# Optimization experiments

Measured on AMD Instinct MI355X. Metric: run time of the kernel, lower is better.

The kernel has to match this reference:

```python
import jax, jax.numpy as jnp
import numpy as np

BETA = 0.25


def setup_inputs() -> dict:
    key = jax.random.key(0)
    k1, k2 = jax.random.split(key)
    z_e = jax.random.normal(k1, (16, 64, 64, 64), dtype=jnp.float32)  # (B, D, H, W)
    embedding = jax.random.normal(k2, (1024, 64), dtype=jnp.float32)  # (K, D)
    return {"z_e": z_e, "embedding": embedding}


def reference(z_e, embedding):
    B, D, H, W = z_e.shape
    # (B, D, H, W) -> (B, H, W, D) -> (N, D)
    flat = jnp.transpose(z_e, (0, 2, 3, 1)).reshape(-1, D)
    # squared L2 distances to codebook: (N, K)
    dist = (jnp.sum(flat * flat, axis=1, keepdims=True)
            + jnp.sum(embedding * embedding, axis=1)
            - 2.0 * flat @ embedding.T)
    indices = jnp.argmin(dist, axis=1)  # (N,)
    z_q_flat = embedding[indices]  # (N, D) gather
    z_q = jnp.transpose(z_q_flat.reshape(B, H, W, D), (0, 3, 1, 2))  # (B, D, H, W)
    codebook_loss = jnp.mean((jax.lax.stop_gradient(z_q) - z_e) ** 2)
    commit_loss = jnp.mean((z_q - jax.lax.stop_gradient(z_e)) ** 2)
    vq_loss = codebook_loss + BETA * commit_loss
    # straight-through estimator
    z_q_st = z_e + jax.lax.stop_gradient(z_q - z_e)
    return (z_q_st, vq_loss, indices.reshape(B, H, W))
```

## Files before the change

kernel.cpp:

```cpp
#include <hip/hip_runtime.h>
#include <math.h>

typedef short  short8 __attribute__((ext_vector_type(8)));
typedef float  f32x4  __attribute__((ext_vector_type(4)));

#define ZQ_ELEMS 4194304
#define KC       1024
#define EPS_HALF 0.005f
#define PXB      128


__device__ inline unsigned short bf16_rne(float f) {
    union { float fv; unsigned u; } a; a.fv = f;
    unsigned r = a.u + 0x7FFFu + ((a.u >> 16) & 1u);
    return (unsigned short)(r >> 16);
}
__device__ inline float bf16_to_f(unsigned short h) {
    union { unsigned u; float fv; } a; a.u = ((unsigned)h) << 16;
    return a.fv;
}
__device__ inline double dpack(float hi, unsigned lo) {
    return __hiloint2double(__float_as_int(hi), (int)lo);
}
__device__ inline float dhi(double d) { return __int_as_float(__double2hiint(d)); }
__device__ inline unsigned dlo(double d) { return (unsigned)__double2loint(d); }

__global__ __launch_bounds__(256) void vq_prep(const float* __restrict__ emb,
        unsigned short* __restrict__ epack, float* __restrict__ enorm,
        int* __restrict__ risky_cnt, float* __restrict__ out) {
    const int k = blockIdx.x * 256 + threadIdx.x;
    if (k == 0) { *risky_cnt = 0; out[ZQ_ELEMS] = 0.f; }
    const float4* e4 = (const float4*)(emb + k * 64);
    float s = 0.f;
#pragma unroll
    for (int j = 0; j < 16; ++j) {
        float4 v = e4[j];
        float vv[4] = {v.x, v.y, v.z, v.w};
        ushort4 hv, lv;
        unsigned short h[4], l[4];
#pragma unroll
        for (int t = 0; t < 4; ++t) {
            s = fmaf(vv[t], vv[t], s);
            h[t] = bf16_rne(vv[t]);
            l[t] = bf16_rne(vv[t] - bf16_to_f(h[t]));
        }
        hv.x = h[0]; hv.y = h[1]; hv.z = h[2]; hv.w = h[3];
        lv.x = l[0]; lv.y = l[1]; lv.z = l[2]; lv.w = l[3];
        *(ushort4*)(epack + k * 128 + j * 4)      = hv;
        *(ushort4*)(epack + k * 128 + 64 + j * 4) = lv;
    }
    enorm[k] = s;
}

__global__ __launch_bounds__(256) void vq_scan(const float* __restrict__ z_e,
        const unsigned short* __restrict__ epack, const float* __restrict__ enorm,
        double* __restrict__ pbest, float* __restrict__ pb2) {
    const int tid  = threadIdx.x;
    const int lane = tid & 63;
    const int col  = lane & 15;
    const int g    = lane >> 4;
    const int wv   = __builtin_amdgcn_readfirstlane(tid >> 6);
    const int pxblock = blockIdx.x >> 2;
    const int grp     = blockIdx.x & 3;
    const int cbase   = grp * 256 + wv * 64;
    const int pblk    = pxblock * PXB;

    __shared__ __align__(16) char smem[32768];
    unsigned short* afrag = (unsigned short*)smem;
    double* mrgB = (double*)smem;
    float*  mrgS = (float*)(smem + 4096);

    {
        const int lp   = tid & 127;
        const int half = tid >> 7;
        const int pg   = pblk + lp;
        const float* zb = z_e + (pg >> 12) * 262144 + (pg & 4095);
        const int sx = (lp & 7) << 3;
#pragma unroll
        for (int s8 = 0; s8 < 4; ++s8) {
            const int d0 = half * 32 + s8 * 8;
            short8 H, L;
#pragma unroll
            for (int j = 0; j < 8; ++j) {
                float v = zb[(d0 + j) * 4096];
                unsigned short h = bf16_rne(v);
                H[j] = (short)h;
                L[j] = (short)bf16_rne(v - bf16_to_f(h));
            }
            const int sw = d0 ^ sx;
            *(short8*)&afrag[lp * 128 + sw]      = H;
            *(short8*)&afrag[lp * 128 + 64 + sw] = L;
        }
    }

    short8 ah[4][2], al[4][2];
    f32x4 enf[4];
    int clo[4][4];
    const int K1 = 1023 - cbase - g * 4;
#pragma unroll
    for (int t = 0; t < 4; ++t) {
        const int code = cbase + t * 16 + col;
        const short8* ph = (const short8*)(epack + code * 128) + g;
        ah[t][0] = ph[0]; ah[t][1] = ph[4];
        al[t][0] = ph[8]; al[t][1] = ph[12];
        const float4 e4 = *(const float4*)(enorm + cbase + t * 16 + g * 4);
        enf[t][0] = -0.5f * e4.x; enf[t][1] = -0.5f * e4.y;
        enf[t][2] = -0.5f * e4.z; enf[t][3] = -0.5f * e4.w;
#pragma unroll
        for (int r = 0; r < 4; ++r) clo[t][r] = K1 - t * 16 - r;
    }
    __syncthreads();

    const f32x4 zero4 = {0.f, 0.f, 0.f, 0.f};
    const int g8 = g * 8;

    double Brun[8];
    float  Srun[8];
#pragma unroll
    for (int it = 0; it < 8; ++it) { Brun[it] = dpack(-INFINITY, 0u); Srun[it] = -INFINITY; }

#pragma unroll
    for (int it = 0; it < 8; ++it) {
        const int lpx = it * 16 + col;
        const int sxp = (lpx & 7) << 3;
        const unsigned short* ap = &afrag[lpx * 128];
        const short8 bh0 = *(const short8*)&ap[(g8        ) ^ sxp];
        const short8 bh1 = *(const short8*)&ap[(32 + g8   ) ^ sxp];
        const short8 bl0 = *(const short8*)&ap[64 + ((g8     ) ^ sxp)];
        const short8 bl1 = *(const short8*)&ap[64 + ((32 + g8) ^ sxp)];

        double B = Brun[it];
        float  S = Srun[it];
#pragma unroll
        for (int t = 0; t < 4; ++t) {
            f32x4 aA, aB;
            aA = __builtin_amdgcn_mfma_f32_16x16x32_bf16(ah[t][0], bh0, enf[t], 0, 0, 0);
            aB = __builtin_amdgcn_mfma_f32_16x16x32_bf16(ah[t][1], bh1, zero4, 0, 0, 0);
            aA = __builtin_amdgcn_mfma_f32_16x16x32_bf16(al[t][0], bh0, aA, 0, 0, 0);
            aB = __builtin_amdgcn_mfma_f32_16x16x32_bf16(al[t][1], bh1, aB, 0, 0, 0);
            aA = __builtin_amdgcn_mfma_f32_16x16x32_bf16(ah[t][0], bl0, aA, 0, 0, 0);
            aB = __builtin_amdgcn_mfma_f32_16x16x32_bf16(ah[t][1], bl1, aB, 0, 0, 0);
#pragma unroll
            for (int r = 0; r < 4; ++r) {
                const float v = aA[r] + aB[r];
                S = __builtin_amdgcn_fmed3f(dhi(B), S, v);
                B = fmax(B, dpack(v, (unsigned)clo[t][r]));
            }
        }
        Brun[it] = B;
        Srun[it] = S;
    }

#pragma unroll
    for (int it = 0; it < 8; ++it) {
        double B = Brun[it];
        float  S = Srun[it];
#pragma unroll
        for (int s = 16; s < 64; s <<= 1) {
            const double ob = __shfl_xor(B, s, 64);
            const float  o2 = __shfl_xor(S, s, 64);
            S = __builtin_amdgcn_fmed3f(dhi(B), dhi(ob), fmaxf(S, o2));
            B = fmax(B, ob);
        }
        Brun[it] = B;
        Srun[it] = S;
    }

    __syncthreads();
    if (g == 0) {
#pragma unroll
        for (int it = 0; it < 8; ++it) {
            mrgB[wv * PXB + it * 16 + col] = Brun[it];
            mrgS[wv * PXB + it * 16 + col] = Srun[it];
        }
    }
    __syncthreads();

    if (tid < PXB) {
        double B = mrgB[tid];
        float  S = mrgS[tid];
#pragma unroll
        for (int w = 1; w < 4; ++w) {
            const double ob = mrgB[w * PXB + tid];
            const float  o2 = mrgS[w * PXB + tid];
            S = __builtin_amdgcn_fmed3f(dhi(B), dhi(ob), fmaxf(S, o2));
            B = fmax(B, ob);
        }
        const int pxg = pblk + tid;
        pbest[grp * 65536 + pxg] = B;
        pb2[grp * 65536 + pxg]   = S;
    }
}

__global__ __launch_bounds__(256) void vq_final(const float* __restrict__ z_e,
        const float* __restrict__ emb, const double* __restrict__ pbest,
        const float* __restrict__ pb2, float* __restrict__ out,
        int* __restrict__ risky_cnt, int* __restrict__ risky) {
    __shared__ float zq[64][65];
    __shared__ int   sidx[64];
    __shared__ float sred[4];
    const int tid  = threadIdx.x;
    const int lane = tid & 63;
    const int w    = __builtin_amdgcn_readfirstlane(tid >> 6);
    const int pblk = blockIdx.x * 64;
    const int batch = pblk >> 12;
    const int hw0   = pblk & 4095;

    if (w == 0) {
        const int px = pblk + lane;
        double B = pbest[px];
        float  S = pb2[px];
#pragma unroll
        for (int gq = 1; gq < 4; ++gq) {
            const double ob = pbest[gq * 65536 + px];
            const float  o2 = pb2[gq * 65536 + px];
            S = __builtin_amdgcn_fmed3f(dhi(B), dhi(ob), fmaxf(S, o2));
            B = fmax(B, ob);
        }
        const int idx = 1023 - (int)dlo(B);
        sidx[lane] = idx;
        out[ZQ_ELEMS + 1 + px] = (float)idx;
        const bool risk = (dhi(B) - S < EPS_HALF);
        const unsigned long long m = __ballot(risk);
        int base = 0;
        if (lane == 0 && m) base = atomicAdd(risky_cnt, __popcll(m));
        base = __shfl(base, 0, 64);
        if (risk) risky[base + __popcll(m & ((1ull << lane) - 1ull))] = px;
    }
    __syncthreads();

#pragma unroll
    for (int i = 0; i < 16; ++i) {
        const int p = w * 16 + i;
        const int k = sidx[p];
        zq[p][lane] = emb[k * 64 + lane];
    }
    __syncthreads();

    const int p4 = (tid & 15) * 4;
    const float* zeb = z_e + batch * 262144 + hw0;
    float* ob = out + batch * 262144 + hw0;
    float ss = 0.f;
#pragma unroll
    for (int it = 0; it < 4; ++it) {
        const int d = (tid >> 4) + it * 16;
        float4 q;
        q.x = zq[p4 + 0][d]; q.y = zq[p4 + 1][d];
        q.z = zq[p4 + 2][d]; q.w = zq[p4 + 3][d];
        const float4 z = *(const float4*)(zeb + d * 4096 + p4);
        *(float4*)(ob + d * 4096 + p4) = q;
        const float e0 = q.x - z.x, e1 = q.y - z.y, e2 = q.z - z.z, e3 = q.w - z.w;
        ss += e0 * e0 + e1 * e1 + e2 * e2 + e3 * e3;
    }
    for (int off = 32; off; off >>= 1) ss += __shfl_down(ss, off, 64);
    if (lane == 0) sred[w] = ss;
    __syncthreads();
    if (tid == 0)
        atomicAdd(out + ZQ_ELEMS,
                  ((sred[0] + sred[1]) + (sred[2] + sred[3])) * (1.25f / (float)ZQ_ELEMS));
}

__global__ __launch_bounds__(256) void vq_fix(const float* __restrict__ z_e,
        const float* __restrict__ emb, float* __restrict__ out,
        const int* __restrict__ cnt, const int* __restrict__ list) {
    const int n = *cnt;
    if ((int)blockIdx.x * 4 >= n) return;
    __shared__ float etile[64][65];
    const int tid  = threadIdx.x;
    const int lane = tid & 63;
    const int wv   = __builtin_amdgcn_readfirstlane(tid >> 6);

    for (int base = blockIdx.x * 4; base < n; base += gridDim.x * 4) {
        const int item = base + wv;
        const bool active = item < n;
        int pix = 0, oldk = 0;
        float f[64];
        if (active) {
            pix = list[item];
            const float* zb = z_e + (pix >> 12) * 262144 + (pix & 4095);
#pragma unroll
            for (int d = 0; d < 64; ++d) f[d] = zb[d * 4096];
            oldk = (int)out[ZQ_ELEMS + 1 + pix];
        }
        double best = INFINITY; int bk = KC;
        double dold = 0.0;
        for (int j = 0; j < 16; ++j) {
            __syncthreads();
#pragma unroll
            for (int i = 0; i < 16; ++i) {
                const int idx = i * 256 + tid;
                etile[idx >> 6][idx & 63] = emb[j * 4096 + idx];
            }
            __syncthreads();
            if (active) {
                const int k = j * 64 + lane;
                double a0 = 0.0, a1 = 0.0;
#pragma unroll
                for (int d = 0; d < 64; d += 2) {
                    const double d0 = (double)f[d]     - (double)etile[lane][d];
                    const double d1 = (double)f[d + 1] - (double)etile[lane][d + 1];
                    a0 = fma(d0, d0, a0);
                    a1 = fma(d1, d1, a1);
                }
                const double acc = a0 + a1;
                if (acc < best || (acc == best && k < bk)) { best = acc; bk = k; }
                if (k == oldk) dold = acc;
            }
        }
        if (active) {
            for (int off = 32; off; off >>= 1) {
                const double ov = __shfl_down(best, off, 64);
                const int    oi = __shfl_down(bk, off, 64);
                if (ov < best || (ov == best && oi < bk)) { best = ov; bk = oi; }
            }
            for (int off = 32; off; off >>= 1) dold += __shfl_down(dold, off, 64);
            bk   = __shfl(bk, 0, 64);
            best = __shfl(best, 0, 64);
            dold = __shfl(dold, 0, 64);
            if (bk != oldk) {
                if (lane == 0) out[ZQ_ELEMS + 1 + pix] = (float)bk;
                out[(pix >> 12) * 262144 + (pix & 4095) + lane * 4096] = emb[bk * 64 + lane];
                if (lane == 0)
                    atomicAdd(out + ZQ_ELEMS,
                              (float)((best - dold) * (1.25 / (double)ZQ_ELEMS)));
            }
        }
    }
}

extern "C" void kernel_launch(void* const* d_in, const int* in_sizes, int n_in,
                              void* d_out, int out_size, void* d_ws, size_t ws_size,
                              hipStream_t stream) {
    const float* z_e = (const float*)d_in[0];
    const float* emb = (const float*)d_in[1];
    float* out = (float*)d_out;
    char* ws = (char*)d_ws;
    unsigned short* epack = (unsigned short*)ws;
    float*  enorm     = (float*)(ws + 262144);
    int*    risky_cnt = (int*)(ws + 266240);
    int*    risky     = (int*)(ws + 270336);
    double* pbest     = (double*)(ws + 524288);
    float*  pb2       = (float*)(ws + 2621440);

    vq_prep<<<4, 256, 0, stream>>>(emb, epack, enorm, risky_cnt, out);
    vq_scan<<<2048, 256, 0, stream>>>(z_e, epack, enorm, pbest, pb2);
    vq_final<<<1024, 256, 0, stream>>>(z_e, emb, pbest, pb2, out, risky_cnt, risky);
    vq_fix<<<512, 256, 0, stream>>>(z_e, emb, out, risky_cnt, risky);
}
```

Before: 90.03 us.

## Fuse scan and finalize kernels, looping over all codebook groups per block

Each block now handles 64 pixels against the full 1024-entry codebook in four sequential passes instead of splitting the codebook across four blocks. This lets the argmin merge, index write, risky-pixel listing, z_q gather, output write and loss reduction run in the same kernel, removing the pbest/pb2 global round trip and one kernel launch. In exchange, each pass reloads codebook fragments into registers, the grid halves to 1024 blocks, and per-block work becomes longer and more serialized.

```diff
diff --git a/kernel.cpp b/kernel.cpp
--- a/kernel.cpp
+++ b/kernel.cpp
@@ -7,7 +7,6 @@
 #define ZQ_ELEMS 4194304
 #define KC       1024
 #define EPS_HALF 0.005f
-#define PXB      128
 
 
 __device__ inline unsigned short bf16_rne(float f) {
@@ -54,31 +53,31 @@
 
 __global__ __launch_bounds__(256) void vq_scan(const float* __restrict__ z_e,
         const unsigned short* __restrict__ epack, const float* __restrict__ enorm,
-        double* __restrict__ pbest, float* __restrict__ pb2) {
+        const float* __restrict__ emb, float* __restrict__ out,
+        int* __restrict__ risky_cnt, int* __restrict__ risky) {
     const int tid  = threadIdx.x;
     const int lane = tid & 63;
     const int col  = lane & 15;
     const int g    = lane >> 4;
     const int wv   = __builtin_amdgcn_readfirstlane(tid >> 6);
-    const int pxblock = blockIdx.x >> 2;
-    const int grp     = blockIdx.x & 3;
-    const int cbase   = grp * 256 + wv * 64;
-    const int pblk    = pxblock * PXB;
-
-    __shared__ __align__(16) char smem[32768];
+    const int pblk = blockIdx.x * 64;
+
+    __shared__ __align__(16) char smem[19456];
     unsigned short* afrag = (unsigned short*)smem;
-    double* mrgB = (double*)smem;
-    float*  mrgS = (float*)(smem + 4096);
+    double* mrgB = (double*)(smem + 16384);
+    float*  mrgS = (float*)(smem + 18432);
+    float (*zq)[65] = (float (*)[65])smem;
+    __shared__ int   sidx[64];
+    __shared__ float sred[4];
 
     {
-        const int lp   = tid & 127;
-        const int half = tid >> 7;
-        const int pg   = pblk + lp;
+        const int lp = tid & 63;
+        const int pg = pblk + lp;
         const float* zb = z_e + (pg >> 12) * 262144 + (pg & 4095);
         const int sx = (lp & 7) << 3;
 #pragma unroll
-        for (int s8 = 0; s8 < 4; ++s8) {
-            const int d0 = half * 32 + s8 * 8;
+        for (int s8 = 0; s8 < 2; ++s8) {
+            const int d0 = wv * 16 + s8 * 8;
             short8 H, L;
 #pragma unroll
             for (int j = 0; j < 8; ++j) {
@@ -92,67 +91,68 @@
             *(short8*)&afrag[lp * 128 + 64 + sw] = L;
         }
     }
-
-    short8 ah[4][2], al[4][2];
-    f32x4 enf[4];
-    int clo[4][4];
-    const int K1 = 1023 - cbase - g * 4;
-#pragma unroll
-    for (int t = 0; t < 4; ++t) {
-        const int code = cbase + t * 16 + col;
-        const short8* ph = (const short8*)(epack + code * 128) + g;
-        ah[t][0] = ph[0]; ah[t][1] = ph[4];
-        al[t][0] = ph[8]; al[t][1] = ph[12];
-        const float4 e4 = *(const float4*)(enorm + cbase + t * 16 + g * 4);
-        enf[t][0] = -0.5f * e4.x; enf[t][1] = -0.5f * e4.y;
-        enf[t][2] = -0.5f * e4.z; enf[t][3] = -0.5f * e4.w;
-#pragma unroll
-        for (int r = 0; r < 4; ++r) clo[t][r] = K1 - t * 16 - r;
-    }
     __syncthreads();
 
     const f32x4 zero4 = {0.f, 0.f, 0.f, 0.f};
     const int g8 = g * 8;
 
-    double Brun[8];
-    float  Srun[8];
-#pragma unroll
-    for (int it = 0; it < 8; ++it) { Brun[it] = dpack(-INFINITY, 0u); Srun[it] = -INFINITY; }
-
-#pragma unroll
-    for (int it = 0; it < 8; ++it) {
-        const int lpx = it * 16 + col;
-        const int sxp = (lpx & 7) << 3;
-        const unsigned short* ap = &afrag[lpx * 128];
-        const short8 bh0 = *(const short8*)&ap[(g8        ) ^ sxp];
-        const short8 bh1 = *(const short8*)&ap[(32 + g8   ) ^ sxp];
-        const short8 bl0 = *(const short8*)&ap[64 + ((g8     ) ^ sxp)];
-        const short8 bl1 = *(const short8*)&ap[64 + ((32 + g8) ^ sxp)];
-
-        double B = Brun[it];
-        float  S = Srun[it];
+    double Brun[4];
+    float  Srun[4];
+#pragma unroll
+    for (int it = 0; it < 4; ++it) { Brun[it] = dpack(-INFINITY, 0u); Srun[it] = -INFINITY; }
+
+#pragma unroll 1
+    for (int pass = 0; pass < 4; ++pass) {
+        const int cbase = pass * 256 + wv * 64;
+        short8 ah[4][2], al[4][2];
+        f32x4 enf[4];
 #pragma unroll
         for (int t = 0; t < 4; ++t) {
-            f32x4 aA, aB;
-            aA = __builtin_amdgcn_mfma_f32_16x16x32_bf16(ah[t][0], bh0, enf[t], 0, 0, 0);
-            aB = __builtin_amdgcn_mfma_f32_16x16x32_bf16(ah[t][1], bh1, zero4, 0, 0, 0);
-            aA = __builtin_amdgcn_mfma_f32_16x16x32_bf16(al[t][0], bh0, aA, 0, 0, 0);
-            aB = __builtin_amdgcn_mfma_f32_16x16x32_bf16(al[t][1], bh1, aB, 0, 0, 0);
-            aA = __builtin_amdgcn_mfma_f32_16x16x32_bf16(ah[t][0], bl0, aA, 0, 0, 0);
-            aB = __builtin_amdgcn_mfma_f32_16x16x32_bf16(ah[t][1], bl1, aB, 0, 0, 0);
-#pragma unroll
-            for (int r = 0; r < 4; ++r) {
-                const float v = aA[r] + aB[r];
-                S = __builtin_amdgcn_fmed3f(dhi(B), S, v);
-                B = fmax(B, dpack(v, (unsigned)clo[t][r]));
-            }
-        }
-        Brun[it] = B;
-        Srun[it] = S;
-    }
-
-#pragma unroll
-    for (int it = 0; it < 8; ++it) {
+            const int code = cbase + t * 16 + col;
+            const short8* ph = (const short8*)(epack + code * 128) + g;
+            ah[t][0] = ph[0]; ah[t][1] = ph[4];
+            al[t][0] = ph[8]; al[t][1] = ph[12];
+            const float4 e4 = *(const float4*)(enorm + cbase + t * 16 + g * 4);
+            enf[t][0] = -0.5f * e4.x; enf[t][1] = -0.5f * e4.y;
+            enf[t][2] = -0.5f * e4.z; enf[t][3] = -0.5f * e4.w;
+        }
+        const int K1 = 1023 - cbase - g * 4;
+
+#pragma unroll
+        for (int it = 0; it < 4; ++it) {
+            const int lpx = it * 16 + col;
+            const int sxp = (lpx & 7) << 3;
+            const unsigned short* ap = &afrag[lpx * 128];
+            const short8 bh0 = *(const short8*)&ap[(g8     ) ^ sxp];
+            const short8 bh1 = *(const short8*)&ap[(32 + g8) ^ sxp];
+            const short8 bl0 = *(const short8*)&ap[64 + ((g8     ) ^ sxp)];
+            const short8 bl1 = *(const short8*)&ap[64 + ((32 + g8) ^ sxp)];
+
+            double B = Brun[it];
+            float  S = Srun[it];
+#pragma unroll
+            for (int t = 0; t < 4; ++t) {
+                f32x4 aA, aB;
+                aA = __builtin_amdgcn_mfma_f32_16x16x32_bf16(ah[t][0], bh0, enf[t], 0, 0, 0);
+                aB = __builtin_amdgcn_mfma_f32_16x16x32_bf16(ah[t][1], bh1, zero4, 0, 0, 0);
+                aA = __builtin_amdgcn_mfma_f32_16x16x32_bf16(al[t][0], bh0, aA, 0, 0, 0);
+                aB = __builtin_amdgcn_mfma_f32_16x16x32_bf16(al[t][1], bh1, aB, 0, 0, 0);
+                aA = __builtin_amdgcn_mfma_f32_16x16x32_bf16(ah[t][0], bl0, aA, 0, 0, 0);
+                aB = __builtin_amdgcn_mfma_f32_16x16x32_bf16(ah[t][1], bl1, aB, 0, 0, 0);
+#pragma unroll
+                for (int r = 0; r < 4; ++r) {
+                    const float v = aA[r] + aB[r];
+                    S = __builtin_amdgcn_fmed3f(dhi(B), S, v);
+                    B = fmax(B, dpack(v, (unsigned)(K1 - t * 16 - r)));
+                }
+            }
+            Brun[it] = B;
+            Srun[it] = S;
+        }
+    }
+
+#pragma unroll
+    for (int it = 0; it < 4; ++it) {
         double B = Brun[it];
         float  S = Srun[it];
 #pragma unroll
@@ -165,78 +165,48 @@
         Brun[it] = B;
         Srun[it] = S;
     }
-
     __syncthreads();
     if (g == 0) {
 #pragma unroll
-        for (int it = 0; it < 8; ++it) {
-            mrgB[wv * PXB + it * 16 + col] = Brun[it];
-            mrgS[wv * PXB + it * 16 + col] = Srun[it];
-        }
-    }
-    __syncthreads();
-
-    if (tid < PXB) {
+        for (int it = 0; it < 4; ++it) {
+            mrgB[wv * 64 + it * 16 + col] = Brun[it];
+            mrgS[wv * 64 + it * 16 + col] = Srun[it];
+        }
+    }
+    __syncthreads();
+
+    if (tid < 64) {
         double B = mrgB[tid];
         float  S = mrgS[tid];
 #pragma unroll
         for (int w = 1; w < 4; ++w) {
-            const double ob = mrgB[w * PXB + tid];
-            const float  o2 = mrgS[w * PXB + tid];
+            const double ob = mrgB[w * 64 + tid];
+            const float  o2 = mrgS[w * 64 + tid];
             S = __builtin_amdgcn_fmed3f(dhi(B), dhi(ob), fmaxf(S, o2));
             B = fmax(B, ob);
         }
-        const int pxg = pblk + tid;
-        pbest[grp * 65536 + pxg] = B;
-        pb2[grp * 65536 + pxg]   = S;
-    }
-}
-
-__global__ __launch_bounds__(256) void vq_final(const float* __restrict__ z_e,
-        const float* __restrict__ emb, const double* __restrict__ pbest,
-        const float* __restrict__ pb2, float* __restrict__ out,
-        int* __restrict__ risky_cnt, int* __restrict__ risky) {
-    __shared__ float zq[64][65];
-    __shared__ int   sidx[64];
-    __shared__ float sred[4];
-    const int tid  = threadIdx.x;
-    const int lane = tid & 63;
-    const int w    = __builtin_amdgcn_readfirstlane(tid >> 6);
-    const int pblk = blockIdx.x * 64;
-    const int batch = pblk >> 12;
-    const int hw0   = pblk & 4095;
-
-    if (w == 0) {
-        const int px = pblk + lane;
-        double B = pbest[px];
-        float  S = pb2[px];
-#pragma unroll
-        for (int gq = 1; gq < 4; ++gq) {
-            const double ob = pbest[gq * 65536 + px];
-            const float  o2 = pb2[gq * 65536 + px];
-            S = __builtin_amdgcn_fmed3f(dhi(B), dhi(ob), fmaxf(S, o2));
-            B = fmax(B, ob);
-        }
         const int idx = 1023 - (int)dlo(B);
-        sidx[lane] = idx;
-        out[ZQ_ELEMS + 1 + px] = (float)idx;
+        sidx[tid] = idx;
+        out[ZQ_ELEMS + 1 + pblk + tid] = (float)idx;
         const bool risk = (dhi(B) - S < EPS_HALF);
         const unsigned long long m = __ballot(risk);
         int base = 0;
         if (lane == 0 && m) base = atomicAdd(risky_cnt, __popcll(m));
         base = __shfl(base, 0, 64);
-        if (risk) risky[base + __popcll(m & ((1ull << lane) - 1ull))] = px;
+        if (risk) risky[base + __popcll(m & ((1ull << lane) - 1ull))] = pblk + tid;
     }
     __syncthreads();
 
 #pragma unroll
     for (int i = 0; i < 16; ++i) {
-        const int p = w * 16 + i;
+        const int p = wv * 16 + i;
         const int k = sidx[p];
         zq[p][lane] = emb[k * 64 + lane];
     }
     __syncthreads();
 
+    const int batch = pblk >> 12;
+    const int hw0   = pblk & 4095;
     const int p4 = (tid & 15) * 4;
     const float* zeb = z_e + batch * 262144 + hw0;
     float* ob = out + batch * 262144 + hw0;
@@ -253,7 +223,7 @@
         ss += e0 * e0 + e1 * e1 + e2 * e2 + e3 * e3;
     }
     for (int off = 32; off; off >>= 1) ss += __shfl_down(ss, off, 64);
-    if (lane == 0) sred[w] = ss;
+    if (lane == 0) sred[wv] = ss;
     __syncthreads();
     if (tid == 0)
         atomicAdd(out + ZQ_ELEMS,
@@ -339,11 +309,8 @@
     float*  enorm     = (float*)(ws + 262144);
     int*    risky_cnt = (int*)(ws + 266240);
     int*    risky     = (int*)(ws + 270336);
-    double* pbest     = (double*)(ws + 524288);
-    float*  pb2       = (float*)(ws + 2621440);
 
     vq_prep<<<4, 256, 0, stream>>>(emb, epack, enorm, risky_cnt, out);
-    vq_scan<<<2048, 256, 0, stream>>>(z_e, epack, enorm, pbest, pb2);
-    vq_final<<<1024, 256, 0, stream>>>(z_e, emb, pbest, pb2, out, risky_cnt, risky);
+    vq_scan<<<1024, 256, 0, stream>>>(z_e, epack, enorm, emb, out, risky_cnt, risky);
     vq_fix<<<512, 256, 0, stream>>>(z_e, emb, out, risky_cnt, risky);
 }
```

New measurement: 78.71 us, median of 2. 1.14x faster.
